# Kernel optimization log

Measured on AMD Instinct MI355X. Metric: run time of the kernel, lower is better.

Reference implementation:

```python
import jax, jax.numpy as jnp
import numpy as np

N_QUBITS = 4
N_LAYERS = 3
N_FEATURES = 64
BATCH = 524288


def setup_inputs() -> dict:
    key = jax.random.key(0)
    k1, k2, k3, k4 = jax.random.split(key, 4)
    x = jax.random.normal(k1, (BATCH, N_FEATURES), jnp.float32)
    # nn.Linear(64, 4) params
    lim = 1.0 / np.sqrt(N_FEATURES)
    W_pre = jax.random.uniform(k2, (N_QUBITS, N_FEATURES), jnp.float32, -lim, lim)
    b_pre = jax.random.uniform(k3, (N_QUBITS,), jnp.float32, -lim, lim)
    # quantum circuit weights: randn * 0.1
    qweights = jax.random.normal(k4, (N_LAYERS, N_QUBITS, 2), jnp.float32) * 0.1
    return {"x": x, "W_pre": W_pre, "b_pre": b_pre, "qweights": qweights}


def _coef(theta, n):
    # reshape scalar or [B] angle to broadcast against [B, 2,..,2] (n-1 trailing dims after slicing)
    return jnp.reshape(theta, (-1,) + (1,) * (n - 1))


def _apply_ry(state, wire, theta):
    # RY(t) = [[cos t/2, -sin t/2], [sin t/2, cos t/2]] applied on `wire`
    n = state.ndim - 1
    s = jnp.moveaxis(state, 1 + wire, -1)
    a, b = s[..., 0], s[..., 1]
    c = _coef(jnp.cos(theta / 2), n)
    sn = _coef(jnp.sin(theta / 2), n)
    out = jnp.stack([c * a - sn * b, sn * a + c * b], axis=-1)
    return jnp.moveaxis(out, -1, 1 + wire)


def _apply_rz(state, wire, theta):
    # RZ(t) = diag(e^{-i t/2}, e^{+i t/2})
    n = state.ndim - 1
    s = jnp.moveaxis(state, 1 + wire, -1)
    half = _coef(theta / 2, n)
    out = jnp.stack([jnp.exp(-1j * half) * s[..., 0],
                     jnp.exp(1j * half) * s[..., 1]], axis=-1)
    return jnp.moveaxis(out, -1, 1 + wire)


def _apply_cnot(state, ctrl, tgt):
    s = jnp.moveaxis(state, (1 + ctrl, 1 + tgt), (-2, -1))
    s = jnp.concatenate([s[..., 0:1, :], s[..., 1:2, ::-1]], axis=-2)
    return jnp.moveaxis(s, (-2, -1), (1 + ctrl, 1 + tgt))


def _circuit(angles, qweights):
    # batched 4-qubit statevector simulation; state shape [B, 2,2,2,2] (wire 0 = MSB)
    B, n = angles.shape
    nl = qweights.shape[0]
    state = jnp.zeros((B,) + (2,) * n, jnp.complex64)
    state = state.at[(slice(None),) + (0,) * n].set(1.0)
    for w in range(n):
        state = _apply_ry(state, w, angles[:, w])
    for l in range(nl):
        for w in range(n):
            state = _apply_ry(state, w, qweights[l, w, 0])
            state = _apply_rz(state, w, qweights[l, w, 1])
        for w in range(n):
            state = _apply_cnot(state, w, (w + 1) % n)
    probs = state.real ** 2 + state.imag ** 2  # [B, 2,2,2,2] float32
    exps = []
    for w in range(n):
        marg = jnp.moveaxis(probs, 1 + w, 1).reshape(B, 2, -1).sum(-1)  # [B, 2]
        exps.append(marg[:, 0] - marg[:, 1])  # <Z_w>
    return jnp.stack(exps, axis=1)  # [B, n]


def reference(x, W_pre, b_pre, qweights):
    angles = jnp.tanh(x @ W_pre.T + b_pre)  # [B, n_qubits]
    return _circuit(angles, qweights).astype(jnp.float32)
```

## Files before the change

### kernel.cpp

```cpp
#include <hip/hip_runtime.h>
#include <cmath>


typedef __attribute__((ext_vector_type(8))) short bf16x8;
typedef __attribute__((ext_vector_type(4))) float f32x4;

__device__ __forceinline__ short f2bf(float f) {
  const unsigned u = __float_as_uint(f);
  return (short)((u + 0x7FFF + ((u >> 16) & 1)) >> 16);
}

__global__ __launch_bounds__(256) void qprep_kernel(
    const float* __restrict__ qw,
    float* __restrict__ A_out)
{
  __shared__ float sre[16][17];
  __shared__ float sim[16][17];
  __shared__ float M[4][16][16];
  const int tid = threadIdx.x;
  const int col = tid >> 4;
  const int u   = tid & 15;

  sre[col][u] = (u == col) ? 1.0f : 0.0f;
  sim[col][u] = 0.0f;
  __syncthreads();

#pragma unroll
  for (int l = 0; l < 3; ++l) {
#pragma unroll
    for (int w = 0; w < 4; ++w) {
      const int mask = 8 >> w;
      float sh, ch, sh2, ch2;
      __sincosf(0.5f * qw[(l * 4 + w) * 2 + 0], &sh, &ch);
      __sincosf(0.5f * qw[(l * 4 + w) * 2 + 1], &sh2, &ch2);
      const int ua = u & ~mask, ub = u | mask;
      const float ar = sre[col][ua], ai = sim[col][ua];
      const float br = sre[col][ub], bi = sim[col][ub];
      __syncthreads();
      float nr, ni;
      if (u & mask) { nr = sh * ar + ch * br; ni = sh * ai + ch * bi; }
      else          { nr = ch * ar - sh * br; ni = ch * ai - sh * bi; }
      float rr, ri;
      if (u & mask) { rr = ch2 * nr - sh2 * ni; ri = ch2 * ni + sh2 * nr; }
      else          { rr = ch2 * nr + sh2 * ni; ri = ch2 * ni - sh2 * nr; }
      sre[col][u] = rr; sim[col][u] = ri;
      __syncthreads();
    }
    int src = u;
    if (src & 1) src ^= 8;
    if (src & 2) src ^= 1;
    if (src & 4) src ^= 2;
    if (src & 8) src ^= 4;
    const float pr = sre[col][src], pi = sim[col][src];
    __syncthreads();
    sre[col][u] = pr; sim[col][u] = pi;
    __syncthreads();
  }

  for (int idx = tid; idx < 1024; idx += 256) {
    const int w = idx >> 8, s = (idx >> 4) & 15, t = idx & 15;
    const int mask = 8 >> w;
    float acc = 0.0f;
#pragma unroll
    for (int uu = 0; uu < 16; ++uu) {
      const float z = (uu & mask) ? -1.0f : 1.0f;
      acc += z * (sre[s][uu] * sre[t][uu] + sim[s][uu] * sim[t][uu]);
    }
    M[w][s][t] = acc;
  }
  __syncthreads();

  for (int idx = tid; idx < 324; idx += 256) {
    const int w = idx & 3, pq = idx >> 2;
    const int p = pq / 9, q = pq % 9;
    const int i0 = p / 3, i1 = p % 3, i2 = q / 3, i3 = q % 3;
    float acc = 0.0f;
#pragma unroll
    for (int comb = 0; comb < 16; ++comb) {
      int s = 0, t = 0;
      float coef = 0.0625f;
      int j;
      j = (comb >> 3) & 1; s |= j << 3; t |= ((i0 == 2) ? (j ^ 1) : j) << 3; if (i0 == 1 && j) coef = -coef;
      j = (comb >> 2) & 1; s |= j << 2; t |= ((i1 == 2) ? (j ^ 1) : j) << 2; if (i1 == 1 && j) coef = -coef;
      j = (comb >> 1) & 1; s |= j << 1; t |= ((i2 == 2) ? (j ^ 1) : j) << 1; if (i2 == 1 && j) coef = -coef;
      j = comb & 1;        s |= j;      t |= ((i3 == 2) ? (j ^ 1) : j);      if (i3 == 1 && j) coef = -coef;
      acc = fmaf(coef, M[w][s][t], acc);
    }
    A_out[idx] = acc;
  }
}

__global__ __launch_bounds__(256)
__attribute__((amdgpu_waves_per_eu(4, 4)))
void qmain_kernel(
    const float* __restrict__ x,
    const float* __restrict__ Wp,
    const float* __restrict__ bp,
    const float4* __restrict__ Aws,
    float* __restrict__ out)
{
  __shared__ float wlds[4][256];

  const int tid  = threadIdx.x;
  const int lane = tid & 63;
  const int wid  = tid >> 6;
  const int arow = lane & 15;
  const int kgrp = lane >> 4;
  float* myld = wlds[wid];

  const size_t wrow0 = ((size_t)blockIdx.x * 4 + wid) * 256;

  bf16x8 wf0, wf1;
#pragma unroll
  for (int j = 0; j < 8; ++j) {
    if (arow < 4) {
      wf0[j] = f2bf(Wp[arow * 64 + 0  + kgrp * 8 + j]);
      wf1[j] = f2bf(Wp[arow * 64 + 32 + kgrp * 8 + j]);
    } else {
      wf0[j] = 0; wf1[j] = 0;
    }
  }
  const f32x4 zero = {0.f, 0.f, 0.f, 0.f};

#pragma unroll
  for (int t = 0; t < 4; ++t) {
    const size_t r0 = wrow0 + (size_t)(t * 64);

#pragma unroll
    for (int m = 0; m < 4; ++m) {
      const float* rp = x + (r0 + (size_t)(m * 16 + arow)) * 64 + kgrp * 8;
      const float4 u0 = *reinterpret_cast<const float4*>(rp);
      const float4 u1 = *reinterpret_cast<const float4*>(rp + 4);
      const float4 u2 = *reinterpret_cast<const float4*>(rp + 32);
      const float4 u3 = *reinterpret_cast<const float4*>(rp + 36);
      bf16x8 af0, af1;
      af0[0] = f2bf(u0.x); af0[1] = f2bf(u0.y); af0[2] = f2bf(u0.z);
      af0[3] = f2bf(u0.w); af0[4] = f2bf(u1.x); af0[5] = f2bf(u1.y);
      af0[6] = f2bf(u1.z); af0[7] = f2bf(u1.w);
      af1[0] = f2bf(u2.x); af1[1] = f2bf(u2.y); af1[2] = f2bf(u2.z);
      af1[3] = f2bf(u2.w); af1[4] = f2bf(u3.x); af1[5] = f2bf(u3.y);
      af1[6] = f2bf(u3.z); af1[7] = f2bf(u3.w);

      f32x4 acc = __builtin_amdgcn_mfma_f32_16x16x32_bf16(af0, wf0, zero, 0, 0, 0);
      acc = __builtin_amdgcn_mfma_f32_16x16x32_bf16(af1, wf1, acc, 0, 0, 0);

      if (arow < 4) {
#pragma unroll
        for (int r = 0; r < 4; ++r)
          myld[(m * 16 + kgrp * 4 + r) * 4 + arow] = acc[r];
      }
    }

    asm volatile("" ::: "memory");

    const float4 ang = *reinterpret_cast<const float4*>(&myld[lane * 4]);
    const float t0 = 1.0f - 2.0f / (__expf(2.0f * (ang.x + bp[0])) + 1.0f);
    const float t1 = 1.0f - 2.0f / (__expf(2.0f * (ang.y + bp[1])) + 1.0f);
    const float t2 = 1.0f - 2.0f / (__expf(2.0f * (ang.z + bp[2])) + 1.0f);
    const float t3 = 1.0f - 2.0f / (__expf(2.0f * (ang.w + bp[3])) + 1.0f);

    float c0, s0, c1, s1, c2, s2, c3, s3;
    __sincosf(t0, &s0, &c0); __sincosf(t1, &s1, &c1);
    __sincosf(t2, &s2, &c2); __sincosf(t3, &s3, &c3);

    const float g[9] = {1.f, c1, s1, c0, c0 * c1, c0 * s1,
                        s0, s0 * c1, s0 * s1};
    const float h[9] = {1.f, c3, s3, c2, c2 * c3, c2 * s3,
                        s2, s2 * c3, s2 * s3};

    float e0 = 0.f, e1 = 0.f, e2 = 0.f, e3 = 0.f;
#pragma unroll
    for (int p = 0; p < 9; ++p) {
#pragma unroll
      for (int q2 = 0; q2 < 9; ++q2) {
        const float4 a4 = Aws[p * 9 + q2];
        const float tt = g[p] * h[q2];
        e0 = fmaf(a4.x, tt, e0); e1 = fmaf(a4.y, tt, e1);
        e2 = fmaf(a4.z, tt, e2); e3 = fmaf(a4.w, tt, e3);
      }
    }
    reinterpret_cast<float4*>(out)[r0 + lane] = make_float4(e0, e1, e2, e3);

    asm volatile("" ::: "memory");
  }
}

extern "C" void kernel_launch(void* const* d_in, const int* in_sizes, int n_in,
                              void* d_out, int out_size, void* d_ws, size_t ws_size,
                              hipStream_t stream) {
  const float* x  = (const float*)d_in[0];
  const float* Wp = (const float*)d_in[1];
  const float* bp = (const float*)d_in[2];
  const float* qw = (const float*)d_in[3];
  float* out = (float*)d_out;
  float* A = (float*)d_ws;
  (void)n_in; (void)out_size; (void)ws_size;

  qprep_kernel<<<1, 256, 0, stream>>>(qw, A);

  const int B = in_sizes[0] / 64;
  qmain_kernel<<<B / 1024, 256, 0, stream>>>(x, Wp, bp,
                                             (const float4*)A, out);
}
```

Before: 40.98 us.

## Halve rows per wave and software-pipeline x loads across MFMA sub-tiles

Each wave now handles 128 rows instead of 256, and the grid doubles to keep the full batch covered. The four-subtile loop becomes a hand-written schedule with two register buffers, so the load of the next x sub-tile is issued before the MFMA on the current one. The load of the second tile's first sub-tile is also hoisted above the first tile's tanh/trig tail. The aim is to hide global load latency in this memory-bound kernel, at the cost of more registers and more blocks.

```diff
diff --git a/kernel.cpp b/kernel.cpp
--- a/kernel.cpp
+++ b/kernel.cpp
@@ -90,6 +90,58 @@
   }
 }
 
+#define LDSUB(V0, V1, V2, V3, R0, M) {                                      \
+  const float* rp_ = x + ((R0) + (size_t)((M) * 16 + arow)) * 64 + kgrp * 8;\
+  V0 = *reinterpret_cast<const float4*>(rp_);                               \
+  V1 = *reinterpret_cast<const float4*>(rp_ + 4);                          \
+  V2 = *reinterpret_cast<const float4*>(rp_ + 32);                         \
+  V3 = *reinterpret_cast<const float4*>(rp_ + 36); }
+
+#define DOMFMA(V0, V1, V2, V3, M) {                                         \
+  bf16x8 af0_, af1_;                                                        \
+  af0_[0] = f2bf(V0.x); af0_[1] = f2bf(V0.y); af0_[2] = f2bf(V0.z);         \
+  af0_[3] = f2bf(V0.w); af0_[4] = f2bf(V1.x); af0_[5] = f2bf(V1.y);         \
+  af0_[6] = f2bf(V1.z); af0_[7] = f2bf(V1.w);                               \
+  af1_[0] = f2bf(V2.x); af1_[1] = f2bf(V2.y); af1_[2] = f2bf(V2.z);         \
+  af1_[3] = f2bf(V2.w); af1_[4] = f2bf(V3.x); af1_[5] = f2bf(V3.y);         \
+  af1_[6] = f2bf(V3.z); af1_[7] = f2bf(V3.w);                               \
+  f32x4 acc_ = __builtin_amdgcn_mfma_f32_16x16x32_bf16(af0_, wf0, zero, 0, 0, 0); \
+  acc_ = __builtin_amdgcn_mfma_f32_16x16x32_bf16(af1_, wf1, acc_, 0, 0, 0); \
+  if (arow < 4) {                                                           \
+    _Pragma("unroll")                                                       \
+    for (int r_ = 0; r_ < 4; ++r_)                                          \
+      myld[((M) * 16 + kgrp * 4 + r_) * 4 + arow] = acc_[r_];               \
+  } }
+
+#define TAIL(R0) {                                                          \
+  asm volatile("" ::: "memory");                                            \
+  const float4 ang = *reinterpret_cast<const float4*>(&myld[lane * 4]);     \
+  const float t0 = 1.0f - 2.0f / (__expf(2.0f * (ang.x + bp[0])) + 1.0f);   \
+  const float t1 = 1.0f - 2.0f / (__expf(2.0f * (ang.y + bp[1])) + 1.0f);   \
+  const float t2 = 1.0f - 2.0f / (__expf(2.0f * (ang.z + bp[2])) + 1.0f);   \
+  const float t3 = 1.0f - 2.0f / (__expf(2.0f * (ang.w + bp[3])) + 1.0f);   \
+  float c0, s0, c1, s1, c2, s2, c3, s3;                                     \
+  __sincosf(t0, &s0, &c0); __sincosf(t1, &s1, &c1);                         \
+  __sincosf(t2, &s2, &c2); __sincosf(t3, &s3, &c3);                         \
+  const float g[9] = {1.f, c1, s1, c0, c0 * c1, c0 * s1,                    \
+                      s0, s0 * c1, s0 * s1};                                \
+  const float h[9] = {1.f, c3, s3, c2, c2 * c3, c2 * s3,                    \
+                      s2, s2 * c3, s2 * s3};                                \
+  float e0 = 0.f, e1 = 0.f, e2 = 0.f, e3 = 0.f;                             \
+  _Pragma("unroll")                                                         \
+  for (int p_ = 0; p_ < 9; ++p_) {                                          \
+    _Pragma("unroll")                                                       \
+    for (int q_ = 0; q_ < 9; ++q_) {                                        \
+      const float4 a4 = Aws[p_ * 9 + q_];                                   \
+      const float tt = g[p_] * h[q_];                                       \
+      e0 = fmaf(a4.x, tt, e0); e1 = fmaf(a4.y, tt, e1);                     \
+      e2 = fmaf(a4.z, tt, e2); e3 = fmaf(a4.w, tt, e3);                     \
+    }                                                                       \
+  }                                                                         \
+  reinterpret_cast<float4*>(out)[(R0) + lane] =                             \
+      make_float4(e0, e1, e2, e3);                                          \
+  asm volatile("" ::: "memory"); }
+
 __global__ __launch_bounds__(256)
 __attribute__((amdgpu_waves_per_eu(4, 4)))
 void qmain_kernel(
@@ -108,7 +160,7 @@
   const int kgrp = lane >> 4;
   float* myld = wlds[wid];
 
-  const size_t wrow0 = ((size_t)blockIdx.x * 4 + wid) * 256;
+  const size_t wrow0 = ((size_t)blockIdx.x * 4 + wid) * 128;
 
   bf16x8 wf0, wf1;
 #pragma unroll
@@ -122,67 +174,27 @@
   }
   const f32x4 zero = {0.f, 0.f, 0.f, 0.f};
 
-#pragma unroll
-  for (int t = 0; t < 4; ++t) {
-    const size_t r0 = wrow0 + (size_t)(t * 64);
-
-#pragma unroll
-    for (int m = 0; m < 4; ++m) {
-      const float* rp = x + (r0 + (size_t)(m * 16 + arow)) * 64 + kgrp * 8;
-      const float4 u0 = *reinterpret_cast<const float4*>(rp);
-      const float4 u1 = *reinterpret_cast<const float4*>(rp + 4);
-      const float4 u2 = *reinterpret_cast<const float4*>(rp + 32);
-      const float4 u3 = *reinterpret_cast<const float4*>(rp + 36);
-      bf16x8 af0, af1;
-      af0[0] = f2bf(u0.x); af0[1] = f2bf(u0.y); af0[2] = f2bf(u0.z);
-      af0[3] = f2bf(u0.w); af0[4] = f2bf(u1.x); af0[5] = f2bf(u1.y);
-      af0[6] = f2bf(u1.z); af0[7] = f2bf(u1.w);
-      af1[0] = f2bf(u2.x); af1[1] = f2bf(u2.y); af1[2] = f2bf(u2.z);
-      af1[3] = f2bf(u2.w); af1[4] = f2bf(u3.x); af1[5] = f2bf(u3.y);
-      af1[6] = f2bf(u3.z); af1[7] = f2bf(u3.w);
-
-      f32x4 acc = __builtin_amdgcn_mfma_f32_16x16x32_bf16(af0, wf0, zero, 0, 0, 0);
-      acc = __builtin_amdgcn_mfma_f32_16x16x32_bf16(af1, wf1, acc, 0, 0, 0);
-
-      if (arow < 4) {
-#pragma unroll
-        for (int r = 0; r < 4; ++r)
-          myld[(m * 16 + kgrp * 4 + r) * 4 + arow] = acc[r];
-      }
-    }
-
-    asm volatile("" ::: "memory");
-
-    const float4 ang = *reinterpret_cast<const float4*>(&myld[lane * 4]);
-    const float t0 = 1.0f - 2.0f / (__expf(2.0f * (ang.x + bp[0])) + 1.0f);
-    const float t1 = 1.0f - 2.0f / (__expf(2.0f * (ang.y + bp[1])) + 1.0f);
-    const float t2 = 1.0f - 2.0f / (__expf(2.0f * (ang.z + bp[2])) + 1.0f);
-    const float t3 = 1.0f - 2.0f / (__expf(2.0f * (ang.w + bp[3])) + 1.0f);
-
-    float c0, s0, c1, s1, c2, s2, c3, s3;
-    __sincosf(t0, &s0, &c0); __sincosf(t1, &s1, &c1);
-    __sincosf(t2, &s2, &c2); __sincosf(t3, &s3, &c3);
-
-    const float g[9] = {1.f, c1, s1, c0, c0 * c1, c0 * s1,
-                        s0, s0 * c1, s0 * s1};
-    const float h[9] = {1.f, c3, s3, c2, c2 * c3, c2 * s3,
-                        s2, s2 * c3, s2 * s3};
-
-    float e0 = 0.f, e1 = 0.f, e2 = 0.f, e3 = 0.f;
-#pragma unroll
-    for (int p = 0; p < 9; ++p) {
-#pragma unroll
-      for (int q2 = 0; q2 < 9; ++q2) {
-        const float4 a4 = Aws[p * 9 + q2];
-        const float tt = g[p] * h[q2];
-        e0 = fmaf(a4.x, tt, e0); e1 = fmaf(a4.y, tt, e1);
-        e2 = fmaf(a4.z, tt, e2); e3 = fmaf(a4.w, tt, e3);
-      }
-    }
-    reinterpret_cast<float4*>(out)[r0 + lane] = make_float4(e0, e1, e2, e3);
-
-    asm volatile("" ::: "memory");
-  }
+  const size_t r0 = wrow0;
+  const size_t r1 = wrow0 + 64;
+
+  float4 ua0, ua1, ua2, ua3, ub0, ub1, ub2, ub3;
+
+  LDSUB(ua0, ua1, ua2, ua3, r0, 0);
+  LDSUB(ub0, ub1, ub2, ub3, r0, 1);
+  DOMFMA(ua0, ua1, ua2, ua3, 0); LDSUB(ua0, ua1, ua2, ua3, r0, 2);
+  DOMFMA(ub0, ub1, ub2, ub3, 1); LDSUB(ub0, ub1, ub2, ub3, r0, 3);
+  DOMFMA(ua0, ua1, ua2, ua3, 2); LDSUB(ua0, ua1, ua2, ua3, r1, 0);
+  DOMFMA(ub0, ub1, ub2, ub3, 3);
+
+  TAIL(r0);
+
+  LDSUB(ub0, ub1, ub2, ub3, r1, 1);
+  DOMFMA(ua0, ua1, ua2, ua3, 0); LDSUB(ua0, ua1, ua2, ua3, r1, 2);
+  DOMFMA(ub0, ub1, ub2, ub3, 1); LDSUB(ub0, ub1, ub2, ub3, r1, 3);
+  DOMFMA(ua0, ua1, ua2, ua3, 2);
+  DOMFMA(ub0, ub1, ub2, ub3, 3);
+
+  TAIL(r1);
 }
 
 extern "C" void kernel_launch(void* const* d_in, const int* in_sizes, int n_in,
@@ -199,6 +211,6 @@
   qprep_kernel<<<1, 256, 0, stream>>>(qw, A);
 
   const int B = in_sizes[0] / 64;
-  qmain_kernel<<<B / 1024, 256, 0, stream>>>(x, Wp, bp,
-                                             (const float4*)A, out);
-}
+  qmain_kernel<<<B / 512, 256, 0, stream>>>(x, Wp, bp,
+                                            (const float4*)A, out);
+}
```

After: 37.38 us. 1.1x faster.

## Split fused kernel into pipelined GEMV and separate circuit-evaluation tail kernel

Applied to the files above, without the earlier changes.

Splits the fused kernel into two. A streaming GEMV kernel software-pipelines the x loads three sub-tiles deep, swaps the MFMA operand order so the 16 result lanes write float4 angles straight to the output buffer, and relaxes the waves-per-EU bound. A second kernel then applies tanh and the quantum expectation polynomial in place. The goal is to keep more loads in flight on the bandwidth-bound x read and to drop the LDS staging. The cost is an extra launch plus an 8 MB write and re-read of the angle buffer.

```diff
diff --git a/kernel.cpp b/kernel.cpp
--- a/kernel.cpp
+++ b/kernel.cpp
@@ -90,25 +90,40 @@
   }
 }
 
+#define LDSUB(V0, V1, V2, V3, S) {                                          \
+  const float* rp_ = x + (wrow0 + (size_t)((S) * 16 + arow)) * 64 + kgrp * 8;\
+  V0 = *reinterpret_cast<const float4*>(rp_);                               \
+  V1 = *reinterpret_cast<const float4*>(rp_ + 4);                           \
+  V2 = *reinterpret_cast<const float4*>(rp_ + 32);                          \
+  V3 = *reinterpret_cast<const float4*>(rp_ + 36); }
+
+#define MFST(V0, V1, V2, V3, S) {                                           \
+  bf16x8 xf0_, xf1_;                                                        \
+  xf0_[0] = f2bf(V0.x); xf0_[1] = f2bf(V0.y); xf0_[2] = f2bf(V0.z);         \
+  xf0_[3] = f2bf(V0.w); xf0_[4] = f2bf(V1.x); xf0_[5] = f2bf(V1.y);         \
+  xf0_[6] = f2bf(V1.z); xf0_[7] = f2bf(V1.w);                               \
+  xf1_[0] = f2bf(V2.x); xf1_[1] = f2bf(V2.y); xf1_[2] = f2bf(V2.z);         \
+  xf1_[3] = f2bf(V2.w); xf1_[4] = f2bf(V3.x); xf1_[5] = f2bf(V3.y);         \
+  xf1_[6] = f2bf(V3.z); xf1_[7] = f2bf(V3.w);                               \
+  f32x4 acc_ = __builtin_amdgcn_mfma_f32_16x16x32_bf16(wf0, xf0_, zero, 0, 0, 0); \
+  acc_ = __builtin_amdgcn_mfma_f32_16x16x32_bf16(wf1, xf1_, acc_, 0, 0, 0); \
+  if (lane < 16)                                                            \
+    reinterpret_cast<float4*>(ang)[wrow0 + (S) * 16 + lane] =               \
+        make_float4(acc_[0], acc_[1], acc_[2], acc_[3]); }
+
 __global__ __launch_bounds__(256)
-__attribute__((amdgpu_waves_per_eu(4, 4)))
-void qmain_kernel(
+__attribute__((amdgpu_waves_per_eu(4, 8)))
+void qgemv_kernel(
     const float* __restrict__ x,
     const float* __restrict__ Wp,
-    const float* __restrict__ bp,
-    const float4* __restrict__ Aws,
-    float* __restrict__ out)
+    float* __restrict__ ang)
 {
-  __shared__ float wlds[4][256];
-
   const int tid  = threadIdx.x;
   const int lane = tid & 63;
   const int wid  = tid >> 6;
   const int arow = lane & 15;
   const int kgrp = lane >> 4;
-  float* myld = wlds[wid];
-
-  const size_t wrow0 = ((size_t)blockIdx.x * 4 + wid) * 256;
+  const size_t wrow0 = ((size_t)blockIdx.x * 4 + wid) * 128;
 
   bf16x8 wf0, wf1;
 #pragma unroll
@@ -122,67 +137,53 @@
   }
   const f32x4 zero = {0.f, 0.f, 0.f, 0.f};
 
-#pragma unroll
-  for (int t = 0; t < 4; ++t) {
-    const size_t r0 = wrow0 + (size_t)(t * 64);
-
-#pragma unroll
-    for (int m = 0; m < 4; ++m) {
-      const float* rp = x + (r0 + (size_t)(m * 16 + arow)) * 64 + kgrp * 8;
-      const float4 u0 = *reinterpret_cast<const float4*>(rp);
-      const float4 u1 = *reinterpret_cast<const float4*>(rp + 4);
-      const float4 u2 = *reinterpret_cast<const float4*>(rp + 32);
-      const float4 u3 = *reinterpret_cast<const float4*>(rp + 36);
-      bf16x8 af0, af1;
-      af0[0] = f2bf(u0.x); af0[1] = f2bf(u0.y); af0[2] = f2bf(u0.z);
-      af0[3] = f2bf(u0.w); af0[4] = f2bf(u1.x); af0[5] = f2bf(u1.y);
-      af0[6] = f2bf(u1.z); af0[7] = f2bf(u1.w);
-      af1[0] = f2bf(u2.x); af1[1] = f2bf(u2.y); af1[2] = f2bf(u2.z);
-      af1[3] = f2bf(u2.w); af1[4] = f2bf(u3.x); af1[5] = f2bf(u3.y);
-      af1[6] = f2bf(u3.z); af1[7] = f2bf(u3.w);
-
-      f32x4 acc = __builtin_amdgcn_mfma_f32_16x16x32_bf16(af0, wf0, zero, 0, 0, 0);
-      acc = __builtin_amdgcn_mfma_f32_16x16x32_bf16(af1, wf1, acc, 0, 0, 0);
-
-      if (arow < 4) {
-#pragma unroll
-        for (int r = 0; r < 4; ++r)
-          myld[(m * 16 + kgrp * 4 + r) * 4 + arow] = acc[r];
-      }
-    }
-
-    asm volatile("" ::: "memory");
-
-    const float4 ang = *reinterpret_cast<const float4*>(&myld[lane * 4]);
-    const float t0 = 1.0f - 2.0f / (__expf(2.0f * (ang.x + bp[0])) + 1.0f);
-    const float t1 = 1.0f - 2.0f / (__expf(2.0f * (ang.y + bp[1])) + 1.0f);
-    const float t2 = 1.0f - 2.0f / (__expf(2.0f * (ang.z + bp[2])) + 1.0f);
-    const float t3 = 1.0f - 2.0f / (__expf(2.0f * (ang.w + bp[3])) + 1.0f);
-
-    float c0, s0, c1, s1, c2, s2, c3, s3;
-    __sincosf(t0, &s0, &c0); __sincosf(t1, &s1, &c1);
-    __sincosf(t2, &s2, &c2); __sincosf(t3, &s3, &c3);
-
-    const float g[9] = {1.f, c1, s1, c0, c0 * c1, c0 * s1,
-                        s0, s0 * c1, s0 * s1};
-    const float h[9] = {1.f, c3, s3, c2, c2 * c3, c2 * s3,
-                        s2, s2 * c3, s2 * s3};
-
-    float e0 = 0.f, e1 = 0.f, e2 = 0.f, e3 = 0.f;
-#pragma unroll
-    for (int p = 0; p < 9; ++p) {
-#pragma unroll
-      for (int q2 = 0; q2 < 9; ++q2) {
-        const float4 a4 = Aws[p * 9 + q2];
-        const float tt = g[p] * h[q2];
-        e0 = fmaf(a4.x, tt, e0); e1 = fmaf(a4.y, tt, e1);
-        e2 = fmaf(a4.z, tt, e2); e3 = fmaf(a4.w, tt, e3);
-      }
-    }
-    reinterpret_cast<float4*>(out)[r0 + lane] = make_float4(e0, e1, e2, e3);
-
-    asm volatile("" ::: "memory");
-  }
+  float4 a0, a1, a2, a3, b0, b1, b2, b3, c0, c1, c2, c3;
+  LDSUB(a0, a1, a2, a3, 0);
+  LDSUB(b0, b1, b2, b3, 1);
+  LDSUB(c0, c1, c2, c3, 2);
+  MFST(a0, a1, a2, a3, 0); LDSUB(a0, a1, a2, a3, 3);
+  MFST(b0, b1, b2, b3, 1); LDSUB(b0, b1, b2, b3, 4);
+  MFST(c0, c1, c2, c3, 2); LDSUB(c0, c1, c2, c3, 5);
+  MFST(a0, a1, a2, a3, 3); LDSUB(a0, a1, a2, a3, 6);
+  MFST(b0, b1, b2, b3, 4); LDSUB(b0, b1, b2, b3, 7);
+  MFST(c0, c1, c2, c3, 5);
+  MFST(a0, a1, a2, a3, 6);
+  MFST(b0, b1, b2, b3, 7);
+}
+
+__global__ __launch_bounds__(256) void qtail_kernel(
+    const float* __restrict__ bp,
+    const float4* __restrict__ Aws,
+    float* __restrict__ io)
+{
+  const size_t idx = (size_t)blockIdx.x * 256 + threadIdx.x;
+  float4* io4 = reinterpret_cast<float4*>(io);
+  const float4 ang = io4[idx];
+
+  const float t0 = 1.0f - 2.0f / (__expf(2.0f * (ang.x + bp[0])) + 1.0f);
+  const float t1 = 1.0f - 2.0f / (__expf(2.0f * (ang.y + bp[1])) + 1.0f);
+  const float t2 = 1.0f - 2.0f / (__expf(2.0f * (ang.z + bp[2])) + 1.0f);
+  const float t3 = 1.0f - 2.0f / (__expf(2.0f * (ang.w + bp[3])) + 1.0f);
+
+  float c0, s0, c1, s1, c2, s2, c3, s3;
+  __sincosf(t0, &s0, &c0); __sincosf(t1, &s1, &c1);
+  __sincosf(t2, &s2, &c2); __sincosf(t3, &s3, &c3);
+
+  const float g[9] = {1.f, c1, s1, c0, c0 * c1, c0 * s1, s0, s0 * c1, s0 * s1};
+  const float h[9] = {1.f, c3, s3, c2, c2 * c3, c2 * s3, s2, s2 * c3, s2 * s3};
+
+  float e0 = 0.f, e1 = 0.f, e2 = 0.f, e3 = 0.f;
+#pragma unroll
+  for (int p = 0; p < 9; ++p) {
+#pragma unroll
+    for (int q = 0; q < 9; ++q) {
+      const float4 a4 = Aws[p * 9 + q];
+      const float tt = g[p] * h[q];
+      e0 = fmaf(a4.x, tt, e0); e1 = fmaf(a4.y, tt, e1);
+      e2 = fmaf(a4.z, tt, e2); e3 = fmaf(a4.w, tt, e3);
+    }
+  }
+  io4[idx] = make_float4(e0, e1, e2, e3);
 }
 
 extern "C" void kernel_launch(void* const* d_in, const int* in_sizes, int n_in,
@@ -199,6 +200,6 @@
   qprep_kernel<<<1, 256, 0, stream>>>(qw, A);
 
   const int B = in_sizes[0] / 64;
-  qmain_kernel<<<B / 1024, 256, 0, stream>>>(x, Wp, bp,
-                                             (const float4*)A, out);
-}
+  qgemv_kernel<<<B / 512, 256, 0, stream>>>(x, Wp, out);
+  qtail_kernel<<<B / 256, 256, 0, stream>>>(bp, (const float4*)A, out);
+}
```

Result: slower. 43.69 us (+6.6%).
